# Kernel tuning notes

Measured on AMD Instinct MI355X. Metric: run time of the kernel, lower is better.

## Reference

```python
import jax, jax.numpy as jnp
import numpy as np

NUM_HEADS = 16
ROPE_THETA = 10000.0


def apply_rope(x, pos):
    # x: (B, H, S, d_k), pos: (B, S) int
    d = x.shape[-1]
    inv_freq = ROPE_THETA ** (-jnp.arange(0, d, 2, dtype=jnp.float32) / d)  # (d/2,)
    ang = pos[:, None, :, None].astype(jnp.float32) * inv_freq  # (B, 1, S, d/2)
    cos, sin = jnp.cos(ang), jnp.sin(ang)
    x1, x2 = x[..., 0::2], x[..., 1::2]
    even = x1 * cos - x2 * sin
    odd = x1 * sin + x2 * cos
    return jnp.stack([even, odd], axis=-1).reshape(x.shape)


def setup_inputs() -> dict:
    key = jax.random.key(0)
    ks = jax.random.split(key, 5)
    B, S, D = 2, 2048, 1024
    sc = 1.0 / np.sqrt(D)
    return {
        "x": jax.random.normal(ks[0], (B, S, D), dtype=jnp.float32),
        "token_positions": jnp.broadcast_to(jnp.arange(S, dtype=jnp.int32), (B, S)),
        "Wq": jax.random.normal(ks[1], (D, D), dtype=jnp.float32) * sc,
        "Wk": jax.random.normal(ks[2], (D, D), dtype=jnp.float32) * sc,
        "Wv": jax.random.normal(ks[3], (D, D), dtype=jnp.float32) * sc,
        "Wo": jax.random.normal(ks[4], (D, D), dtype=jnp.float32) * sc,
    }


def reference(x, token_positions, Wq, Wk, Wv, Wo):
    B, S, D = x.shape
    H = NUM_HEADS
    dk = D // H
    # bias-free Linear: y = x @ W.T  (W: (out, in))
    def split_heads(t):
        return t.reshape(B, S, H, dk).transpose(0, 2, 1, 3)  # (B, H, S, dk)
    q = split_heads(x @ Wq.T)
    k = split_heads(x @ Wk.T)
    v = split_heads(x @ Wv.T)
    q = apply_rope(q, token_positions)
    k = apply_rope(k, token_positions)
    scores = jnp.einsum("bhqd,bhkd->bhqk", q, k) / jnp.sqrt(jnp.float32(dk))
    causal = jnp.tril(jnp.ones((S, S), dtype=bool))
    scores = jnp.where(causal, scores, jnp.float32(-1e9))
    attn = jax.nn.softmax(scores, axis=-1)
    out = jnp.einsum("bhqk,bhkd->bhqd", attn, v)  # (B, H, S, dk)
    out = out.transpose(0, 2, 1, 3).reshape(B, S, D)
    return out @ Wo.T
```

## Files before the change

### kernel.cpp

```cpp
#include <hip/hip_runtime.h>
#include <math.h>

using bf_t = unsigned short;
typedef short s16x4 __attribute__((ext_vector_type(4)));
typedef short s16x8 __attribute__((ext_vector_type(8)));
typedef float f32x4 __attribute__((ext_vector_type(4)));

__device__ __forceinline__ bf_t f2bf(float f) {
  unsigned u = __float_as_uint(f);
  u += 0x7FFFu + ((u >> 16) & 1u);
  return (bf_t)(u >> 16);
}
__device__ __forceinline__ float bf2f(bf_t h) {
  return __uint_as_float(((unsigned)h) << 16);
}

union V8 { s16x8 v; s16x4 h[2]; };
__device__ __forceinline__ s16x8 ld_frag(const bf_t* p) {
  V8 u;
  u.h[0] = *(const s16x4*)p;
  u.h[1] = *(const s16x4*)(p + 16);
  return u.v;
}

#define MFMA(A, B, C) __builtin_amdgcn_mfma_f32_16x16x32_bf16((A), (B), (C), 0, 0, 0)

__global__ void cvt_kernel(const float* __restrict__ in, bf_t* __restrict__ out, int n4) {
  int i = blockIdx.x * blockDim.x + threadIdx.x;
  if (i >= n4) return;
  float4 v = ((const float4*)in)[i];
  ushort4 o;
  o.x = f2bf(v.x); o.y = f2bf(v.y); o.z = f2bf(v.z); o.w = f2bf(v.w);
  ((ushort4*)out)[i] = o;
}

template <int EPI>
__global__ __launch_bounds__(256) void gemm_kernel(
    const bf_t* __restrict__ A, const bf_t* __restrict__ Bw,
    float* __restrict__ Cf,
    bf_t* __restrict__ Qb, bf_t* __restrict__ Kb, bf_t* __restrict__ Vt,
    int M, int N, int K) {
  constexpr int BKP = 40;
  __shared__ bf_t As[128 * BKP];
  __shared__ bf_t Bs[128 * BKP];
  const int t = threadIdx.x;
  const int lane = t & 63;
  const int w = t >> 6;
  const int wr = w >> 1, wc = w & 1;
  const int col = lane & 15;
  const int kg = lane >> 4;
  const int m0 = blockIdx.y * 128;
  const int n0 = blockIdx.x * 128;

  f32x4 acc[4][4] = {};

  for (int k0 = 0; k0 < K; k0 += 32) {
#pragma unroll
    for (int p = 0; p < 2; ++p) {
      int idx = t + p * 256;
      int row = idx >> 2;
      int kk = (idx & 3) << 3;
      *(s16x8*)&As[row * BKP + kk] = *(const s16x8*)&A[(size_t)(m0 + row) * K + k0 + kk];
      *(s16x8*)&Bs[row * BKP + kk] = *(const s16x8*)&Bw[(size_t)(n0 + row) * K + k0 + kk];
    }
    __syncthreads();
    s16x8 af[4], bfg[4];
#pragma unroll
    for (int mi = 0; mi < 4; ++mi)
      af[mi] = ld_frag(&As[(wr * 64 + mi * 16 + col) * BKP + kg * 4]);
#pragma unroll
    for (int ni = 0; ni < 4; ++ni)
      bfg[ni] = ld_frag(&Bs[(wc * 64 + ni * 16 + col) * BKP + kg * 4]);
#pragma unroll
    for (int mi = 0; mi < 4; ++mi)
#pragma unroll
      for (int ni = 0; ni < 4; ++ni)
        acc[mi][ni] = MFMA(af[mi], bfg[ni], acc[mi][ni]);
    __syncthreads();
  }

#pragma unroll
  for (int mi = 0; mi < 4; ++mi)
#pragma unroll
    for (int ni = 0; ni < 4; ++ni)
#pragma unroll
      for (int r = 0; r < 4; ++r) {
        int gm = m0 + wr * 64 + mi * 16 + kg * 4 + r;
        int gn = n0 + wc * 64 + ni * 16 + col;
        float v = acc[mi][ni][r];
        if constexpr (EPI == 0) {
          int which = gn >> 10;
          int wn = gn & 1023;
          int h = wn >> 6, d = wn & 63;
          int b = gm >> 11, s = gm & 2047;
          size_t hb = (size_t)(b * 16 + h);
          if (which == 0)
            Qb[(hb * 2048 + s) * 64 + d] = f2bf(v);
          else if (which == 1)
            Kb[(hb * 2048 + s) * 64 + d] = f2bf(v);
          else
            Vt[(hb * 64 + d) * 2048 + s] = f2bf(v);
        } else {
          Cf[(size_t)gm * N + gn] = v;
        }
      }
}

__global__ void rope_kernel(bf_t* __restrict__ Qb, bf_t* __restrict__ Kb,
                            const int* __restrict__ pos, int total) {
  int i = blockIdx.x * blockDim.x + threadIdx.x;
  if (i >= total) return;
  int ip = i & 31;
  int s = (i >> 5) & 2047;
  int bh = i >> 16;
  int b = bh >> 4;
  float p = (float)pos[b * 2048 + s];
  float ang = p * exp2f(-(float)ip * 0.41524101186f);
  float sv, cv;
  sincosf(ang, &sv, &cv);
  size_t base = ((size_t)bh * 2048 + s) * 64 + ip * 2;
  {
    unsigned u = *(const unsigned*)&Qb[base];
    float x1 = bf2f((bf_t)(u & 0xFFFF)), x2 = bf2f((bf_t)(u >> 16));
    unsigned o = (unsigned)f2bf(x1 * cv - x2 * sv) | ((unsigned)f2bf(x1 * sv + x2 * cv) << 16);
    *(unsigned*)&Qb[base] = o;
  }
  {
    unsigned u = *(const unsigned*)&Kb[base];
    float x1 = bf2f((bf_t)(u & 0xFFFF)), x2 = bf2f((bf_t)(u >> 16));
    unsigned o = (unsigned)f2bf(x1 * cv - x2 * sv) | ((unsigned)f2bf(x1 * sv + x2 * cv) << 16);
    *(unsigned*)&Kb[base] = o;
  }
}

__global__ __launch_bounds__(64) void attn_kernel(const bf_t* __restrict__ Qb,
                                                  const bf_t* __restrict__ Kb,
                                                  const bf_t* __restrict__ Vt,
                                                  bf_t* __restrict__ AO) {
  const int lane = threadIdx.x & 63;
  const int col = lane & 15;
  const int kg = lane >> 4;
  const int bh = blockIdx.y;
  const int q0 = blockIdx.x * 64;
  const bf_t* Qp = Qb + (size_t)bh * 2048 * 64;
  const bf_t* Kp = Kb + (size_t)bh * 2048 * 64;
  const bf_t* Vp = Vt + (size_t)bh * 64 * 2048;

  __shared__ bf_t Pl[64 * 40];

  s16x8 qf[4][2];
#pragma unroll
  for (int mi = 0; mi < 4; ++mi)
#pragma unroll
    for (int ks = 0; ks < 2; ++ks)
      qf[mi][ks] = ld_frag(Qp + (size_t)(q0 + mi * 16 + col) * 64 + ks * 32 + kg * 4);

  f32x4 o[4][4] = {};
  float mrun[4][4], lrun[4][4];
#pragma unroll
  for (int mi = 0; mi < 4; ++mi)
#pragma unroll
    for (int r = 0; r < 4; ++r) {
      mrun[mi][r] = -INFINITY;
      lrun[mi][r] = 0.0f;
    }

  for (int kb = 0; kb < q0 + 64; kb += 32) {
    s16x8 kf[2][2];
#pragma unroll
    for (int nk = 0; nk < 2; ++nk)
#pragma unroll
      for (int ks = 0; ks < 2; ++ks)
        kf[nk][ks] = ld_frag(Kp + (size_t)(kb + nk * 16 + col) * 64 + ks * 32 + kg * 4);

    f32x4 sc[4][2] = {};
#pragma unroll
    for (int mi = 0; mi < 4; ++mi)
#pragma unroll
      for (int nk = 0; nk < 2; ++nk)
#pragma unroll
        for (int ks = 0; ks < 2; ++ks)
          sc[mi][nk] = MFMA(qf[mi][ks], kf[nk][ks], sc[mi][nk]);

    const int k0g = kb + col, k1g = kb + 16 + col;
#pragma unroll
    for (int mi = 0; mi < 4; ++mi)
#pragma unroll
      for (int r = 0; r < 4; ++r) {
        int qg = q0 + mi * 16 + kg * 4 + r;
        float s0 = (k0g <= qg) ? sc[mi][0][r] * 0.125f : -INFINITY;
        float s1 = (k1g <= qg) ? sc[mi][1][r] * 0.125f : -INFINITY;
        float mx = fmaxf(s0, s1);
        mx = fmaxf(mx, __shfl_xor(mx, 1));
        mx = fmaxf(mx, __shfl_xor(mx, 2));
        mx = fmaxf(mx, __shfl_xor(mx, 4));
        mx = fmaxf(mx, __shfl_xor(mx, 8));
        float mold = mrun[mi][r];
        float mn = fmaxf(mold, mx);
        float a = __expf(mold - mn);
        float e0 = __expf(s0 - mn);
        float e1 = __expf(s1 - mn);
        sc[mi][0][r] = e0;
        sc[mi][1][r] = e1;
        float rs = e0 + e1;
        rs += __shfl_xor(rs, 1);
        rs += __shfl_xor(rs, 2);
        rs += __shfl_xor(rs, 4);
        rs += __shfl_xor(rs, 8);
        lrun[mi][r] = lrun[mi][r] * a + rs;
        mrun[mi][r] = mn;
#pragma unroll
        for (int ni = 0; ni < 4; ++ni) o[mi][ni][r] *= a;
      }

    __syncthreads();
#pragma unroll
    for (int mi = 0; mi < 4; ++mi)
#pragma unroll
      for (int nk = 0; nk < 2; ++nk)
#pragma unroll
        for (int r = 0; r < 4; ++r)
          Pl[(mi * 16 + kg * 4 + r) * 40 + nk * 16 + col] = f2bf(sc[mi][nk][r]);
    __syncthreads();

    s16x8 pa[4], vf[4];
#pragma unroll
    for (int mi = 0; mi < 4; ++mi) pa[mi] = ld_frag(&Pl[(mi * 16 + col) * 40 + kg * 4]);
#pragma unroll
    for (int ni = 0; ni < 4; ++ni)
      vf[ni] = ld_frag(Vp + (size_t)(ni * 16 + col) * 2048 + kb + kg * 4);
#pragma unroll
    for (int mi = 0; mi < 4; ++mi)
#pragma unroll
      for (int ni = 0; ni < 4; ++ni) o[mi][ni] = MFMA(pa[mi], vf[ni], o[mi][ni]);
  }

  const int b = bh >> 4, h = bh & 15;
#pragma unroll
  for (int mi = 0; mi < 4; ++mi)
#pragma unroll
    for (int r = 0; r < 4; ++r) {
      float inv = 1.0f / lrun[mi][r];
      int qg = q0 + mi * 16 + kg * 4 + r;
#pragma unroll
      for (int ni = 0; ni < 4; ++ni)
        AO[((size_t)b * 2048 + qg) * 1024 + h * 64 + ni * 16 + col] =
            f2bf(o[mi][ni][r] * inv);
    }
}

extern "C" void kernel_launch(void* const* d_in, const int* in_sizes, int n_in,
                              void* d_out, int out_size, void* d_ws, size_t ws_size,
                              hipStream_t stream) {
  const float* x = (const float*)d_in[0];
  const int* pos = (const int*)d_in[1];
  const float* Wq = (const float*)d_in[2];
  const float* Wk = (const float*)d_in[3];
  const float* Wv = (const float*)d_in[4];
  const float* Wo = (const float*)d_in[5];
  float* out = (float*)d_out;

  char* ws = (char*)d_ws;
  bf_t* xb    = (bf_t*)(ws);
  bf_t* Wqkvb = (bf_t*)(ws + 8388608);
  bf_t* Wob   = (bf_t*)(ws + 14680064);
  bf_t* Qb    = (bf_t*)(ws + 16777216);
  bf_t* Kb    = (bf_t*)(ws + 25165824);
  bf_t* Vt    = (bf_t*)(ws + 33554432);
  bf_t* AO    = (bf_t*)(ws + 41943040);

  cvt_kernel<<<4096, 256, 0, stream>>>(x, xb, 1048576);
  cvt_kernel<<<1024, 256, 0, stream>>>(Wq, Wqkvb, 262144);
  cvt_kernel<<<1024, 256, 0, stream>>>(Wk, Wqkvb + 1048576, 262144);
  cvt_kernel<<<1024, 256, 0, stream>>>(Wv, Wqkvb + 2097152, 262144);
  cvt_kernel<<<1024, 256, 0, stream>>>(Wo, Wob, 262144);

  gemm_kernel<0><<<dim3(24, 32), 256, 0, stream>>>(xb, Wqkvb, nullptr, Qb, Kb, Vt,
                                                   4096, 3072, 1024);
  rope_kernel<<<8192, 256, 0, stream>>>(Qb, Kb, pos, 2097152);
  attn_kernel<<<dim3(32, 32), 64, 0, stream>>>(Qb, Kb, Vt, AO);
  gemm_kernel<1><<<dim3(8, 32), 256, 0, stream>>>(AO, Wob, out, nullptr, nullptr, nullptr,
                                                  4096, 1024, 1024);
}
```

Measured before the change: 397.7 us.

## Split attention KV range across four waves and merge partial softmax results

The attention kernel goes from one wave per 64-query block to four waves. Each wave handles an interleaved quarter of the key blocks with a private P buffer, so the per-iteration block barriers are gone. Partial outputs are merged through shared-memory atomics using the online-softmax max/sum rescaling. Query blocks are launched longest-first (reversed order) to balance the causal workload. Fragment loads now read 8 contiguous bf16 values instead of two 4-wide halves; this changes the K-index mapping consistently for both operands. The cost is extra shared memory, atomics and barriers in the merge step, plus a guard for waves that see no valid keys.

```diff
diff --git a/kernel.cpp b/kernel.cpp
--- a/kernel.cpp
+++ b/kernel.cpp
@@ -15,12 +15,8 @@
   return __uint_as_float(((unsigned)h) << 16);
 }
 
-union V8 { s16x8 v; s16x4 h[2]; };
 __device__ __forceinline__ s16x8 ld_frag(const bf_t* p) {
-  V8 u;
-  u.h[0] = *(const s16x4*)p;
-  u.h[1] = *(const s16x4*)(p + 16);
-  return u.v;
+  return *(const s16x8*)p;
 }
 
 #define MFMA(A, B, C) __builtin_amdgcn_mfma_f32_16x16x32_bf16((A), (B), (C), 0, 0, 0)
@@ -67,10 +63,10 @@
     s16x8 af[4], bfg[4];
 #pragma unroll
     for (int mi = 0; mi < 4; ++mi)
-      af[mi] = ld_frag(&As[(wr * 64 + mi * 16 + col) * BKP + kg * 4]);
+      af[mi] = ld_frag(&As[(wr * 64 + mi * 16 + col) * BKP + kg * 8]);
 #pragma unroll
     for (int ni = 0; ni < 4; ++ni)
-      bfg[ni] = ld_frag(&Bs[(wc * 64 + ni * 16 + col) * BKP + kg * 4]);
+      bfg[ni] = ld_frag(&Bs[(wc * 64 + ni * 16 + col) * BKP + kg * 8]);
 #pragma unroll
     for (int mi = 0; mi < 4; ++mi)
 #pragma unroll
@@ -133,27 +129,33 @@
   }
 }
 
-__global__ __launch_bounds__(64) void attn_kernel(const bf_t* __restrict__ Qb,
-                                                  const bf_t* __restrict__ Kb,
-                                                  const bf_t* __restrict__ Vt,
-                                                  bf_t* __restrict__ AO) {
-  const int lane = threadIdx.x & 63;
+__global__ __launch_bounds__(256) void attn_kernel(const bf_t* __restrict__ Qb,
+                                                   const bf_t* __restrict__ Kb,
+                                                   const bf_t* __restrict__ Vt,
+                                                   bf_t* __restrict__ AO) {
+  const int t = threadIdx.x;
+  const int lane = t & 63;
+  const int w = t >> 6;
   const int col = lane & 15;
   const int kg = lane >> 4;
   const int bh = blockIdx.y;
-  const int q0 = blockIdx.x * 64;
+  const int q0 = ((int)gridDim.x - 1 - (int)blockIdx.x) * 64;
   const bf_t* Qp = Qb + (size_t)bh * 2048 * 64;
   const bf_t* Kp = Kb + (size_t)bh * 2048 * 64;
   const bf_t* Vp = Vt + (size_t)bh * 64 * 2048;
 
-  __shared__ bf_t Pl[64 * 40];
+  __shared__ char sh[22528];
+  bf_t* Plw = (bf_t*)sh + w * 2560;
+  float* ocomb = (float*)sh;
+  float* mw = (float*)(sh + 20480);
+  float* lw = (float*)(sh + 21504);
 
   s16x8 qf[4][2];
 #pragma unroll
   for (int mi = 0; mi < 4; ++mi)
 #pragma unroll
     for (int ks = 0; ks < 2; ++ks)
-      qf[mi][ks] = ld_frag(Qp + (size_t)(q0 + mi * 16 + col) * 64 + ks * 32 + kg * 4);
+      qf[mi][ks] = ld_frag(Qp + (size_t)(q0 + mi * 16 + col) * 64 + ks * 32 + kg * 8);
 
   f32x4 o[4][4] = {};
   float mrun[4][4], lrun[4][4];
@@ -165,13 +167,13 @@
       lrun[mi][r] = 0.0f;
     }
 
-  for (int kb = 0; kb < q0 + 64; kb += 32) {
+  for (int kb = w * 32; kb < q0 + 64; kb += 128) {
     s16x8 kf[2][2];
 #pragma unroll
     for (int nk = 0; nk < 2; ++nk)
 #pragma unroll
       for (int ks = 0; ks < 2; ++ks)
-        kf[nk][ks] = ld_frag(Kp + (size_t)(kb + nk * 16 + col) * 64 + ks * 32 + kg * 4);
+        kf[nk][ks] = ld_frag(Kp + (size_t)(kb + nk * 16 + col) * 64 + ks * 32 + kg * 8);
 
     f32x4 sc[4][2] = {};
 #pragma unroll
@@ -197,9 +199,10 @@
         mx = fmaxf(mx, __shfl_xor(mx, 8));
         float mold = mrun[mi][r];
         float mn = fmaxf(mold, mx);
-        float a = __expf(mold - mn);
-        float e0 = __expf(s0 - mn);
-        float e1 = __expf(s1 - mn);
+        float mnc = fmaxf(mn, -1e30f);
+        float a = __expf(mold - mnc);
+        float e0 = __expf(s0 - mnc);
+        float e1 = __expf(s1 - mnc);
         sc[mi][0][r] = e0;
         sc[mi][1][r] = e1;
         float rs = e0 + e1;
@@ -213,40 +216,73 @@
         for (int ni = 0; ni < 4; ++ni) o[mi][ni][r] *= a;
       }
 
-    __syncthreads();
 #pragma unroll
     for (int mi = 0; mi < 4; ++mi)
 #pragma unroll
       for (int nk = 0; nk < 2; ++nk)
 #pragma unroll
         for (int r = 0; r < 4; ++r)
-          Pl[(mi * 16 + kg * 4 + r) * 40 + nk * 16 + col] = f2bf(sc[mi][nk][r]);
-    __syncthreads();
+          Plw[(mi * 16 + kg * 4 + r) * 40 + nk * 16 + col] = f2bf(sc[mi][nk][r]);
 
     s16x8 pa[4], vf[4];
 #pragma unroll
-    for (int mi = 0; mi < 4; ++mi) pa[mi] = ld_frag(&Pl[(mi * 16 + col) * 40 + kg * 4]);
+    for (int mi = 0; mi < 4; ++mi) pa[mi] = ld_frag(&Plw[(mi * 16 + col) * 40 + kg * 8]);
 #pragma unroll
     for (int ni = 0; ni < 4; ++ni)
-      vf[ni] = ld_frag(Vp + (size_t)(ni * 16 + col) * 2048 + kb + kg * 4);
+      vf[ni] = ld_frag(Vp + (size_t)(ni * 16 + col) * 2048 + kb + kg * 8);
 #pragma unroll
     for (int mi = 0; mi < 4; ++mi)
 #pragma unroll
       for (int ni = 0; ni < 4; ++ni) o[mi][ni] = MFMA(pa[mi], vf[ni], o[mi][ni]);
   }
 
+  if (col == 0) {
+#pragma unroll
+    for (int mi = 0; mi < 4; ++mi)
+#pragma unroll
+      for (int r = 0; r < 4; ++r) {
+        int row = mi * 16 + kg * 4 + r;
+        mw[w * 64 + row] = mrun[mi][r];
+        lw[w * 64 + row] = lrun[mi][r];
+      }
+  }
+  __syncthreads();
+
+  for (int i = t; i < 64 * 65; i += 256) ocomb[i] = 0.0f;
+  __syncthreads();
+
+#pragma unroll
+  for (int mi = 0; mi < 4; ++mi)
+#pragma unroll
+    for (int r = 0; r < 4; ++r) {
+      int row = mi * 16 + kg * 4 + r;
+      float ms = fmaxf(fmaxf(mw[row], mw[64 + row]), fmaxf(mw[128 + row], mw[192 + row]));
+      float mo = mrun[mi][r];
+      float s = (mo == -INFINITY) ? 0.0f : __expf(mo - ms);
+#pragma unroll
+      for (int ni = 0; ni < 4; ++ni)
+        atomicAdd(&ocomb[row * 65 + ni * 16 + col], o[mi][ni][r] * s);
+    }
+  __syncthreads();
+
   const int b = bh >> 4, h = bh & 15;
 #pragma unroll
-  for (int mi = 0; mi < 4; ++mi)
-#pragma unroll
-    for (int r = 0; r < 4; ++r) {
-      float inv = 1.0f / lrun[mi][r];
-      int qg = q0 + mi * 16 + kg * 4 + r;
-#pragma unroll
-      for (int ni = 0; ni < 4; ++ni)
-        AO[((size_t)b * 2048 + qg) * 1024 + h * 64 + ni * 16 + col] =
-            f2bf(o[mi][ni][r] * inv);
+  for (int r = 0; r < 4; ++r) {
+    int row = w * 16 + kg * 4 + r;
+    float ms = fmaxf(fmaxf(mw[row], mw[64 + row]), fmaxf(mw[128 + row], mw[192 + row]));
+    float ls = 0.0f;
+#pragma unroll
+    for (int w2 = 0; w2 < 4; ++w2) {
+      float mv = mw[w2 * 64 + row];
+      ls += (mv == -INFINITY) ? 0.0f : lw[w2 * 64 + row] * __expf(mv - ms);
     }
+    float inv = 1.0f / ls;
+    int qg = q0 + row;
+#pragma unroll
+    for (int ni = 0; ni < 4; ++ni)
+      AO[((size_t)b * 2048 + qg) * 1024 + h * 64 + ni * 16 + col] =
+          f2bf(ocomb[row * 65 + ni * 16 + col] * inv);
+  }
 }
 
 extern "C" void kernel_launch(void* const* d_in, const int* in_sizes, int n_in,
@@ -278,7 +314,7 @@
   gemm_kernel<0><<<dim3(24, 32), 256, 0, stream>>>(xb, Wqkvb, nullptr, Qb, Kb, Vt,
                                                    4096, 3072, 1024);
   rope_kernel<<<8192, 256, 0, stream>>>(Qb, Kb, pos, 2097152);
-  attn_kernel<<<dim3(32, 32), 64, 0, stream>>>(Qb, Kb, Vt, AO);
+  attn_kernel<<<dim3(32, 32), 256, 0, stream>>>(Qb, Kb, Vt, AO);
   gemm_kernel<1><<<dim3(8, 32), 256, 0, stream>>>(AO, Wob, out, nullptr, nullptr, nullptr,
                                                   4096, 1024, 1024);
 }
```

New measurement: 512.4 us. +28.9%, slower.
